# Kernel tuning notes

Measured on AMD Instinct MI355X. Metric: run time of the kernel, lower is better.

The kernel has to match this reference:

```python
import jax, jax.numpy as jnp
import numpy as np

HIDDEN = 2048
N_HEADS = 32
N_KV_HEADS = 8
N_GROUPS = N_HEADS // N_KV_HEADS  # 4
HEAD_DIM = HIDDEN // N_HEADS      # 64
BATCH, SEQ = 2, 2048


def setup_inputs() -> dict:
    key = jax.random.key(0)
    ks = jax.random.split(key, 5)
    s = 0.02
    return {
        "x": jax.random.normal(ks[0], (BATCH, SEQ, HIDDEN), dtype=jnp.float32),
        "Wq": jax.random.normal(ks[1], (HIDDEN, HIDDEN), dtype=jnp.float32) * s,
        "Wk": jax.random.normal(ks[2], (N_KV_HEADS * HEAD_DIM, HIDDEN), dtype=jnp.float32) * s,
        "Wv": jax.random.normal(ks[3], (N_KV_HEADS * HEAD_DIM, HIDDEN), dtype=jnp.float32) * s,
        "Wo": jax.random.normal(ks[4], (HIDDEN, HIDDEN), dtype=jnp.float32) * s,
    }


def reference(x, Wq, Wk, Wv, Wo):
    b, s, _ = x.shape
    # Projections (nn.Linear: y = x @ W.T)
    q = (x @ Wq.T).reshape(b, s, N_KV_HEADS, N_GROUPS, HEAD_DIM)  # group heads by kv head
    k = (x @ Wk.T).reshape(b, s, N_KV_HEADS, HEAD_DIM)
    v = (x @ Wv.T).reshape(b, s, N_KV_HEADS, HEAD_DIM)
    scale = 1.0 / jnp.sqrt(jnp.asarray(HEAD_DIM, dtype=x.dtype))
    # Grouped scores: equivalent to repeat_interleave of K over groups
    scores = jnp.einsum('bqhgd,bkhd->bhgqk', q, k) * scale  # [b, kvh, g, s, s]
    causal_mask = jnp.triu(jnp.ones((s, s), dtype=bool), k=1)
    scores = jnp.where(causal_mask, -jnp.inf, scores)
    attn = jax.nn.softmax(scores, axis=-1)
    out = jnp.einsum('bhgqk,bkhd->bqhgd', attn, v)  # [b, s, kvh, g, hd]
    out = out.reshape(b, s, HIDDEN)
    return out @ Wo.T
```

## Files before the change

kernel.cpp:

```cpp
#include <hip/hip_runtime.h>

#define HIDDEN 2048
#define NHEADS 32
#define NKV 8
#define HD 64
#define BATCH 2
#define SEQ 2048
#define MROWS (BATCH*SEQ)
#define KVDIM (NKV*HD)
#define QKVN (HIDDEN + 2*KVDIM)

typedef __bf16 bf16x8 __attribute__((ext_vector_type(8)));
typedef __bf16 bf16x4 __attribute__((ext_vector_type(4)));
typedef float f32x4 __attribute__((ext_vector_type(4)));

__device__ inline f32x4 mfma32(bf16x8 a, bf16x8 b, f32x4 c) {
    return __builtin_amdgcn_mfma_f32_16x16x32_bf16(a, b, c, 0, 0, 0);
}

__device__ inline void gld16(const __bf16* g, __bf16* l) {
    __builtin_amdgcn_global_load_lds((const __attribute__((address_space(1))) void*)g,
                                     (__attribute__((address_space(3))) void*)l, 16, 0, 0);
}

__global__ __launch_bounds__(256) void cast_all(const float* __restrict__ x,
                                                const float* __restrict__ wq,
                                                const float* __restrict__ wk,
                                                const float* __restrict__ wv,
                                                const float* __restrict__ wo,
                                                __bf16* __restrict__ xb,
                                                __bf16* __restrict__ wqkv,
                                                __bf16* __restrict__ wob,
                                                float qscale) {
    int blk = blockIdx.x;
    const float* src; __bf16* dst; float sc = 1.0f; size_t off;
    if (blk < 8192)        { src = x;  dst = xb;   off = (size_t)blk * 1024; }
    else if (blk < 12288)  { src = wq; dst = wqkv; off = (size_t)(blk - 8192) * 1024; sc = qscale; }
    else if (blk < 13312)  { src = wk; dst = wqkv + (size_t)HIDDEN * HIDDEN; off = (size_t)(blk - 12288) * 1024; }
    else if (blk < 14336)  { src = wv; dst = wqkv + (size_t)(HIDDEN + KVDIM) * HIDDEN; off = (size_t)(blk - 13312) * 1024; }
    else                   { src = wo; dst = wob;  off = (size_t)(blk - 14336) * 1024; }
    size_t i4 = off + (size_t)threadIdx.x * 4;
    float4 f = *(const float4*)(src + i4);
    dst[i4 + 0] = (__bf16)(f.x * sc);
    dst[i4 + 1] = (__bf16)(f.y * sc);
    dst[i4 + 2] = (__bf16)(f.z * sc);
    dst[i4 + 3] = (__bf16)(f.w * sc);
}

__device__ inline void store_val(__bf16* C, size_t idx, float v) { C[idx] = (__bf16)v; }
__device__ inline void store_val(float* C, size_t idx, float v) { C[idx] = v; }

template <typename OutT>
__global__ __launch_bounds__(256) void gemm128(const __bf16* __restrict__ A,
                                               const __bf16* __restrict__ B,
                                               OutT* __restrict__ C,
                                               int M, int N, int K) {
    __shared__ __bf16 As[2][128][32];
    __shared__ __bf16 Bs[2][128][32];
    const int tid  = threadIdx.x;
    const int lane = tid & 63;
    const int w    = tid >> 6;
    const int col  = lane & 15;
    const int quad = lane >> 4;
    const int m0 = blockIdx.y * 128;
    const int n0 = blockIdx.x * 128;
    const int wm = (w >> 1) * 64;
    const int wn = (w & 1) * 64;

    f32x4 acc[4][4];
    #pragma unroll
    for (int i = 0; i < 4; i++)
        #pragma unroll
        for (int j = 0; j < 4; j++) acc[i][j] = (f32x4){0.f,0.f,0.f,0.f};

    const int lrow = lane >> 2;
    const int lcol = (lane & 3) * 8;

    auto stage = [&](int k0, int buf) {
        #pragma unroll
        for (int c = 0; c < 4; c++) {
            int chunk = w * 4 + c;
            if (chunk < 8) {
                const __bf16* g = A + (size_t)(m0 + chunk*16 + lrow) * K + k0 + lcol;
                gld16(g, &As[buf][chunk*16][0]);
            } else {
                int bc = chunk - 8;
                const __bf16* g = B + (size_t)(n0 + bc*16 + lrow) * K + k0 + lcol;
                gld16(g, &Bs[buf][bc*16][0]);
            }
        }
    };

    const int nk = K / 32;
    stage(0, 0);
    for (int ki = 0; ki < nk; ki++) {
        const int buf = ki & 1;
        __syncthreads();
        if (ki + 1 < nk) stage((ki + 1) * 32, buf ^ 1);

        bf16x8 af[4], bfr[4];
        #pragma unroll
        for (int i = 0; i < 4; i++) af[i]  = *(const bf16x8*)&As[buf][wm + i*16 + col][quad*8];
        #pragma unroll
        for (int j = 0; j < 4; j++) bfr[j] = *(const bf16x8*)&Bs[buf][wn + j*16 + col][quad*8];
        #pragma unroll
        for (int i = 0; i < 4; i++)
            #pragma unroll
            for (int j = 0; j < 4; j++)
                acc[i][j] = __builtin_amdgcn_mfma_f32_16x16x32_bf16(af[i], bfr[j], acc[i][j], 0, 0, 0);
    }

    #pragma unroll
    for (int i = 0; i < 4; i++) {
        #pragma unroll
        for (int r = 0; r < 4; r++) {
            int mrow = m0 + wm + i*16 + quad*4 + r;
            size_t base = (size_t)mrow * N + n0 + wn;
            #pragma unroll
            for (int j = 0; j < 4; j++)
                store_val(C, base + j*16 + col, acc[i][j][r]);
        }
    }
}

__global__ __launch_bounds__(256) void transpose_v(const __bf16* __restrict__ QKV,
                                                   __bf16* __restrict__ VT) {
    __shared__ __bf16 tile[64][72];
    const int r0 = blockIdx.x * 64;
    const int s0 = blockIdx.y * 64;
    const int t  = threadIdx.x;
    #pragma unroll
    for (int cc = 0; cc < 2; cc++) {
        int c = t + cc * 256;
        int i = c >> 3;
        int j8 = (c & 7) * 8;
        bf16x8 v = *(const bf16x8*)(QKV + (size_t)(s0 + i) * QKVN + (HIDDEN + KVDIM) + r0 + j8);
        *(bf16x8*)&tile[i][j8] = v;
    }
    __syncthreads();
    #pragma unroll
    for (int cc = 0; cc < 2; cc++) {
        int c = t + cc * 256;
        int d = c >> 3;
        int m = c & 7;
        bf16x8 vv;
        #pragma unroll
        for (int tt = 0; tt < 8; tt++) {
            int sl = (m >> 2) * 32 + (tt >> 2) * 16 + (m & 3) * 4 + (tt & 3);
            vv[tt] = tile[sl][d];
        }
        *(bf16x8*)(VT + (size_t)(r0 + d) * MROWS + s0 + m * 8) = vv;
    }
}

__global__ __launch_bounds__(256) void flash_attn(const __bf16* __restrict__ QKV,
                                                  const __bf16* __restrict__ VT,
                                                  __bf16* __restrict__ O) {
    const int bid  = blockIdx.x;
    const int t    = 31 - (bid >> 6);
    const int head = (bid >> 1) & 31;
    const int b    = bid & 1;
    const int kvh  = head >> 2;
    const int tid  = threadIdx.x;
    const int lane = tid & 63;
    const int w    = tid >> 6;
    const int col  = lane & 15;
    const int quad = lane >> 4;

    const int qb   = t * 64 + w * 16;
    const int n32  = (t + 1) * 2;

    __shared__ __bf16 Ks[3][2][32][32];
    __shared__ __bf16 Vs[3][64][32];

    const size_t qO = (size_t)(b * SEQ + qb + col) * QKVN + head * HD;
    bf16x8 aq0 = *(const bf16x8*)(QKV + qO + quad * 8);
    bf16x8 aq1 = *(const bf16x8*)(QKV + qO + 32 + quad * 8);

    bf16x8 ones8;
    #pragma unroll
    for (int j = 0; j < 8; j++) ones8[j] = (__bf16)1.0f;

    f32x4 o[4];
    #pragma unroll
    for (int dn = 0; dn < 4; dn++) o[dn] = (f32x4){0.f,0.f,0.f,0.f};
    f32x4 lsum = (f32x4){0.f,0.f,0.f,0.f};

    const int lrow = lane >> 2;
    const int srcc8 = (((lane & 3) ^ (lrow & 3)) * 8);
    const int swz   = (quad ^ (col & 3)) * 8;
    const size_t bS = (size_t)b * SEQ;

    const __bf16 *g0, *g1;
    size_t gstep;
    if (w < 2) {
        g0 = QKV + (bS + lrow) * QKVN + HIDDEN + kvh * HD + w * 32 + srcc8;
        g1 = g0 + (size_t)16 * QKVN;
        gstep = (size_t)32 * QKVN;
    } else {
        g0 = VT + (size_t)(kvh * HD + (w - 2) * 32 + lrow) * MROWS + bS + (lane & 3) * 8;
        g1 = g0 + (size_t)16 * MROWS;
        gstep = 32;
    }

    auto stage = [&](int sb) {
        if (w < 2) {
            gld16(g0, &Ks[sb][w][0][0]);
            gld16(g1, &Ks[sb][w][16][0]);
        } else {
            gld16(g0, &Vs[sb][(w - 2) * 32][0]);
            gld16(g1, &Vs[sb][(w - 2) * 32 + 16][0]);
        }
        g0 += gstep; g1 += gstep;
    };

    stage(0);
    stage(1);
    int cur = 0, nx2 = 2;
    for (int kt = 0; kt < n32; kt++) {
        const int kbase = kt * 32;
        if (kt + 1 < n32) { __asm__ volatile("s_waitcnt vmcnt(2)" ::: "memory"); }
        else              { __asm__ volatile("s_waitcnt vmcnt(0)" ::: "memory"); }
        __builtin_amdgcn_s_barrier();
        __asm__ volatile("" ::: "memory");
        if (kt + 2 < n32) stage(nx2);

        f32x4 s[2];
        s[0] = (f32x4){0.f,0.f,0.f,0.f};
        s[1] = (f32x4){0.f,0.f,0.f,0.f};
        __builtin_amdgcn_s_setprio(1);
        #pragma unroll
        for (int j = 0; j < 2; j++) {
            bf16x8 bk0 = *(const bf16x8*)&Ks[cur][0][j*16 + col][swz];
            bf16x8 bk1 = *(const bf16x8*)&Ks[cur][1][j*16 + col][swz];
            s[j] = mfma32(bk0, aq0, s[j]);
            s[j] = mfma32(bk1, aq1, s[j]);
        }
        __builtin_amdgcn_s_setprio(0);

        if (kt >= n32 - 2) {
            #pragma unroll
            for (int j = 0; j < 2; j++)
                #pragma unroll
                for (int r = 0; r < 4; r++)
                    if (kbase + j*16 + quad*4 + r > qb + col) s[j][r] = -1e30f;
        }

        bf16x8 pa;
        #pragma unroll
        for (int j = 0; j < 2; j++)
            #pragma unroll
            for (int r = 0; r < 4; r++)
                pa[j*4 + r] = (__bf16)__builtin_amdgcn_exp2f(s[j][r]);

        __builtin_amdgcn_s_setprio(1);
        lsum = mfma32(pa, ones8, lsum);
        #pragma unroll
        for (int dn = 0; dn < 4; dn++) {
            bf16x8 bv = *(const bf16x8*)&Vs[cur][dn*16 + col][quad*8];
            o[dn] = mfma32(pa, bv, o[dn]);
        }
        __builtin_amdgcn_s_setprio(0);

        cur = (cur == 2) ? 0 : cur + 1;
        nx2 = (nx2 == 2) ? 0 : nx2 + 1;
    }

    #pragma unroll
    for (int r = 0; r < 4; r++) {
        float inv = 1.0f / lsum[r];
        __bf16* op = O + (size_t)(b * SEQ + qb + quad*4 + r) * HIDDEN + head * HD;
        #pragma unroll
        for (int dn = 0; dn < 4; dn++)
            op[dn*16 + col] = (__bf16)(o[dn][r] * inv);
    }
}

extern "C" void kernel_launch(void* const* d_in, const int* in_sizes, int n_in,
                              void* d_out, int out_size, void* d_ws, size_t ws_size,
                              hipStream_t stream) {
    const float* x  = (const float*)d_in[0];
    const float* Wq = (const float*)d_in[1];
    const float* Wk = (const float*)d_in[2];
    const float* Wv = (const float*)d_in[3];
    const float* Wo = (const float*)d_in[4];
    float* out = (float*)d_out;

    __bf16* p    = (__bf16*)d_ws;
    __bf16* xb   = p; p += (size_t)MROWS * HIDDEN;
    __bf16* wqkv = p; p += (size_t)QKVN * HIDDEN;
    __bf16* wob  = p; p += (size_t)HIDDEN * HIDDEN;
    __bf16* qkv  = p; p += (size_t)MROWS * QKVN;
    __bf16* vt   = p; p += (size_t)KVDIM * MROWS;
    __bf16* aob  = xb;

    const float qscale = 0.125f * 1.4426950408889634f;
    cast_all<<<18432, 256, 0, stream>>>(x, Wq, Wk, Wv, Wo, xb, wqkv, wob, qscale);

    dim3 blk(256);
    gemm128<__bf16><<<dim3(QKVN/128, MROWS/128), blk, 0, stream>>>(xb, wqkv, qkv, MROWS, QKVN, HIDDEN);
    transpose_v<<<dim3(KVDIM/64, MROWS/64), blk, 0, stream>>>(qkv, vt);
    flash_attn<<<BATCH * NHEADS * (SEQ/64), blk, 0, stream>>>(qkv, vt, aob);
    gemm128<float><<<dim3(HIDDEN/128, MROWS/128), blk, 0, stream>>>(aob, wob, out, MROWS, HIDDEN, HIDDEN);
}
```

Before: 283.9 us.

## Add 256x256 pipelined GEMM with 8 waves for QKV projection

Adds a new gemm256 kernel for the fused QKV projection. It uses 256x256 output tiles, 512 threads, double-buffered LDS filled by direct global-to-LDS loads with XOR swizzling, and an interleaved schedule of LDS reads, MFMA and prefetch issues with explicit waitcnt, barriers and s_setprio. Larger tiles raise reuse per loaded byte and the software pipeline is meant to hide load latency. The grid becomes small (12x16 = 192 blocks), which may underfill the GPU, and the hand-tuned vmcnt counts carry correctness risk.

```diff
diff --git a/kernel.cpp b/kernel.cpp
--- a/kernel.cpp
+++ b/kernel.cpp
@@ -123,6 +123,131 @@
     }
 }
 
+__global__ __launch_bounds__(512, 2) void gemm256(const __bf16* __restrict__ A,
+                                                  const __bf16* __restrict__ B,
+                                                  __bf16* __restrict__ C,
+                                                  int M, int N, int K) {
+    __shared__ __bf16 As[2][256][64];
+    __shared__ __bf16 Bs[2][256][64];
+    const int tid  = threadIdx.x;
+    const int lane = tid & 63;
+    const int w    = tid >> 6;
+    const int wr   = w >> 2;
+    const int wc   = w & 3;
+    const int col  = lane & 15;
+    const int quad = lane >> 4;
+    const int m0 = blockIdx.y * 256;
+    const int n0 = blockIdx.x * 256;
+    const int nk = K >> 6;
+
+    f32x4 acc[8][4];
+    #pragma unroll
+    for (int i = 0; i < 8; i++)
+        #pragma unroll
+        for (int j = 0; j < 4; j++) acc[i][j] = (f32x4){0.f,0.f,0.f,0.f};
+
+    bf16x8 afr[4][2];
+    bf16x8 bfr[4][2];
+
+    const int r8 = lane >> 3, c8 = lane & 7;
+    const __bf16* pA0 = A + (size_t)(m0 + w*16 +     r8) * K + ((c8 ^ quad) * 8);
+    const __bf16* pA1 = A + (size_t)(m0 + w*16 + 8 + r8) * K + ((c8 ^ (4 + quad)) * 8);
+    const __bf16* pB0 = B + (size_t)(n0 + w*16 +     r8) * K + ((c8 ^ quad) * 8);
+    const __bf16* pB1 = B + (size_t)(n0 + w*16 + 8 + r8) * K + ((c8 ^ (4 + quad)) * 8);
+    const int ldsrow = w * 16;
+    const int rsw = col >> 1;
+
+#define G2_BAR()   { __asm__ volatile("" ::: "memory"); __builtin_amdgcn_s_barrier(); __asm__ volatile("" ::: "memory"); }
+#define G2_LGKM0() { __asm__ volatile("s_waitcnt lgkmcnt(0)" ::: "memory"); __builtin_amdgcn_sched_barrier(0); }
+#define G2_ISSUE(tile, sel) do {                                                             \
+    int _t = (tile);                                                                         \
+    if (_t < nk) {                                                                           \
+        int _b = _t & 1; size_t _ko = (size_t)_t * 64;                                       \
+        if      ((sel) == 0) { gld16(pA0 + _ko, &As[_b][ldsrow][0]);                         \
+                               gld16(pA1 + _ko, &As[_b][ldsrow + 8][0]); }                   \
+        else if ((sel) == 1) { gld16(pA0 + (size_t)128*K + _ko, &As[_b][128 + ldsrow][0]);   \
+                               gld16(pA1 + (size_t)128*K + _ko, &As[_b][128 + ldsrow + 8][0]); } \
+        else if ((sel) == 2) { gld16(pB0 + _ko, &Bs[_b][ldsrow][0]);                         \
+                               gld16(pB1 + _ko, &Bs[_b][ldsrow + 8][0]); }                   \
+        else                 { gld16(pB0 + (size_t)128*K + _ko, &Bs[_b][128 + ldsrow][0]);   \
+                               gld16(pB1 + (size_t)128*K + _ko, &Bs[_b][128 + ldsrow + 8][0]); } \
+    } } while (0)
+#define G2_LDA(mh) {                                                                         \
+    _Pragma("unroll")                                                                        \
+    for (int ii = 0; ii < 4; ii++) {                                                         \
+        const __bf16* _rp = &As[buf][wr*128 + ((mh)*4 + ii)*16 + col][0];                    \
+        _Pragma("unroll")                                                                    \
+        for (int kk = 0; kk < 2; kk++)                                                       \
+            afr[ii][kk] = *(const bf16x8*)(_rp + (((kk*4 + quad) ^ rsw) * 8));               \
+    } }
+#define G2_LDB(nh) {                                                                         \
+    _Pragma("unroll")                                                                        \
+    for (int jj = 0; jj < 2; jj++) {                                                         \
+        const __bf16* _rp = &Bs[buf][wc*64 + ((nh)*2 + jj)*16 + col][0];                     \
+        _Pragma("unroll")                                                                    \
+        for (int kk = 0; kk < 2; kk++)                                                       \
+            bfr[(nh)*2 + jj][kk] = *(const bf16x8*)(_rp + (((kk*4 + quad) ^ rsw) * 8));      \
+    } }
+#define G2_MM(mh, nh) {                                                                      \
+    __builtin_amdgcn_s_setprio(1);                                                           \
+    _Pragma("unroll")                                                                        \
+    for (int ii = 0; ii < 4; ii++)                                                           \
+        _Pragma("unroll")                                                                    \
+        for (int jj = 0; jj < 2; jj++)                                                       \
+            _Pragma("unroll")                                                                \
+            for (int kk = 0; kk < 2; kk++)                                                   \
+                acc[(mh)*4 + ii][(nh)*2 + jj] =                                              \
+                    mfma32(afr[ii][kk], bfr[(nh)*2 + jj][kk], acc[(mh)*4 + ii][(nh)*2 + jj]); \
+    __builtin_amdgcn_s_setprio(0); }
+
+    G2_ISSUE(0, 0); G2_ISSUE(0, 1); G2_ISSUE(0, 2); G2_ISSUE(0, 3);
+    G2_ISSUE(1, 0); G2_ISSUE(1, 2); G2_ISSUE(1, 3);
+    __asm__ volatile("s_waitcnt vmcnt(6)" ::: "memory");
+    G2_BAR();
+
+    for (int t = 0; t < nk; ++t) {
+        const int buf = t & 1;
+        G2_LDA(0); G2_LDB(0);
+        G2_ISSUE(t + 1, 1);
+        G2_BAR(); G2_LGKM0();
+        G2_MM(0, 0);
+        G2_BAR();
+        G2_LDB(1);
+        G2_BAR(); G2_LGKM0();
+        G2_MM(0, 1);
+        G2_BAR();
+        G2_LDA(1);
+        G2_ISSUE(t + 2, 2);
+        G2_BAR(); G2_LGKM0();
+        G2_MM(1, 1);
+        G2_BAR();
+        G2_ISSUE(t + 2, 0);
+        G2_ISSUE(t + 2, 3);
+        G2_BAR(); G2_LGKM0();
+        G2_MM(1, 0);
+        if (t + 3 <= nk) { __asm__ volatile("s_waitcnt vmcnt(6)" ::: "memory"); }
+        else             { __asm__ volatile("s_waitcnt vmcnt(0)" ::: "memory"); }
+        G2_BAR();
+    }
+
+    #pragma unroll
+    for (int i16 = 0; i16 < 8; i16++) {
+        #pragma unroll
+        for (int r = 0; r < 4; r++) {
+            size_t base = (size_t)(m0 + wr*128 + i16*16 + quad*4 + r) * N + n0 + wc*64;
+            #pragma unroll
+            for (int j16 = 0; j16 < 4; j16++)
+                C[base + j16*16 + col] = (__bf16)acc[i16][j16][r];
+        }
+    }
+#undef G2_BAR
+#undef G2_LGKM0
+#undef G2_ISSUE
+#undef G2_LDA
+#undef G2_LDB
+#undef G2_MM
+}
+
 __global__ __launch_bounds__(256) void transpose_v(const __bf16* __restrict__ QKV,
                                                    __bf16* __restrict__ VT) {
     __shared__ __bf16 tile[64][72];
@@ -297,9 +422,8 @@
     const float qscale = 0.125f * 1.4426950408889634f;
     cast_all<<<18432, 256, 0, stream>>>(x, Wq, Wk, Wv, Wo, xb, wqkv, wob, qscale);
 
-    dim3 blk(256);
-    gemm128<__bf16><<<dim3(QKVN/128, MROWS/128), blk, 0, stream>>>(xb, wqkv, qkv, MROWS, QKVN, HIDDEN);
-    transpose_v<<<dim3(KVDIM/64, MROWS/64), blk, 0, stream>>>(qkv, vt);
-    flash_attn<<<BATCH * NHEADS * (SEQ/64), blk, 0, stream>>>(qkv, vt, aob);
-    gemm128<float><<<dim3(HIDDEN/128, MROWS/128), blk, 0, stream>>>(aob, wob, out, MROWS, HIDDEN, HIDDEN);
-}
+    gemm256<<<dim3(QKVN/256, MROWS/256), 512, 0, stream>>>(xb, wqkv, qkv, MROWS, QKVN, HIDDEN);
+    transpose_v<<<dim3(KVDIM/64, MROWS/64), dim3(256), 0, stream>>>(qkv, vt);
+    flash_attn<<<BATCH * NHEADS * (SEQ/64), dim3(256), 0, stream>>>(qkv, vt, aob);
+    gemm128<float><<<dim3(HIDDEN/128, MROWS/128), dim3(256), 0, stream>>>(aob, wob, out, MROWS, HIDDEN, HIDDEN);
+}
```

After: 280.0 us. About the same (-1.4%).

## Use 256x192-tile double-buffered GEMM for the fused QKV projection

Applied to the files above, without the earlier changes.

Adds a new 512-thread GEMM kernel for the QKV projection. It uses 256x192 output tiles, double-buffered LDS filled by direct global-to-LDS loads, XOR-swizzled LDS reads, and MFMA issue interleaved with register prefetch under s_setprio. The larger tile raises arithmetic intensity and the software pipelining overlaps loads with MFMAs, aiming to speed up the QKV GEMM. QKVN=3072 divides evenly by 192 into 16 column blocks, giving 256 blocks in total. The cost is heavier register and LDS use per block.

```diff
diff --git a/kernel.cpp b/kernel.cpp
--- a/kernel.cpp
+++ b/kernel.cpp
@@ -123,6 +123,145 @@
     }
 }
 
+__global__ __launch_bounds__(512, 2) void gemm256(const __bf16* __restrict__ A,
+                                                  const __bf16* __restrict__ B,
+                                                  __bf16* __restrict__ C,
+                                                  int M, int N, int K) {
+    __shared__ __bf16 As[2][256][64];
+    __shared__ __bf16 Bs[2][192][64];
+    const int tid  = threadIdx.x;
+    const int lane = tid & 63;
+    const int w    = tid >> 6;
+    const int wr   = w >> 2;
+    const int wc   = w & 3;
+    const int col  = lane & 15;
+    const int quad = lane >> 4;
+    const int m0 = blockIdx.y * 256;
+    const int n0 = blockIdx.x * 192;
+    const int nk = K >> 6;
+
+    f32x4 acc[8][3];
+    #pragma unroll
+    for (int i = 0; i < 8; i++)
+        #pragma unroll
+        for (int j = 0; j < 3; j++) acc[i][j] = (f32x4){0.f,0.f,0.f,0.f};
+
+    bf16x8 amh0[4][2];
+    bf16x8 amh1[4][2];
+    bf16x8 b01[2][2];
+    bf16x8 b2v[2];
+
+    const int r8 = lane >> 3, c8 = lane & 7;
+    const __bf16* pA0 = A + (size_t)(m0 + w*16 +     r8) * K + ((c8 ^ quad) * 8);
+    const __bf16* pA1 = A + (size_t)(m0 + w*16 + 8 + r8) * K + ((c8 ^ (4 + quad)) * 8);
+    const __bf16* pB  = B + (size_t)(n0 + w*8 +      r8) * K + ((c8 ^ ((w & 1) * 4 + quad)) * 8);
+    const int rsw = col >> 1;
+
+    auto issue = [&](int tt) {
+        if (tt < nk) {
+            int b = tt & 1; size_t ko = (size_t)tt * 64;
+            gld16(pA0 + ko,                  &As[b][w*16][0]);
+            gld16(pA1 + ko,                  &As[b][w*16 + 8][0]);
+            gld16(pA0 + (size_t)128*K + ko,  &As[b][128 + w*16][0]);
+            gld16(pA1 + (size_t)128*K + ko,  &As[b][128 + w*16 + 8][0]);
+            gld16(pB + ko,                   &Bs[b][w*8][0]);
+            gld16(pB + (size_t)64*K + ko,    &Bs[b][64 + w*8][0]);
+            gld16(pB + (size_t)128*K + ko,   &Bs[b][128 + w*8][0]);
+        }
+    };
+    auto rdA = [&](bf16x8 (&dst)[4][2], int b, int rowbase) {
+        #pragma unroll
+        for (int i = 0; i < 4; i++) {
+            const __bf16* rp = &As[b][rowbase + i*16 + col][0];
+            #pragma unroll
+            for (int kk = 0; kk < 2; kk++)
+                dst[i][kk] = *(const bf16x8*)(rp + (((kk*4 + quad) ^ rsw) * 8));
+        }
+    };
+    auto rdB01 = [&](int b) {
+        #pragma unroll
+        for (int j = 0; j < 2; j++) {
+            const __bf16* rp = &Bs[b][wc*48 + j*16 + col][0];
+            #pragma unroll
+            for (int kk = 0; kk < 2; kk++)
+                b01[j][kk] = *(const bf16x8*)(rp + (((kk*4 + quad) ^ rsw) * 8));
+        }
+    };
+
+    issue(0); issue(1);
+    __asm__ volatile("s_waitcnt vmcnt(7)" ::: "memory");
+    __builtin_amdgcn_s_barrier();
+    __asm__ volatile("" ::: "memory");
+    rdA(amh0, 0, wr*128);
+    rdB01(0);
+
+    for (int t = 0; t < nk; ++t) {
+        const int buf = t & 1;
+        {
+            const __bf16* rp = &Bs[buf][wc*48 + 32 + col][0];
+            #pragma unroll
+            for (int kk = 0; kk < 2; kk++)
+                b2v[kk] = *(const bf16x8*)(rp + (((kk*4 + quad) ^ rsw) * 8));
+        }
+        __builtin_amdgcn_s_setprio(1);
+        #pragma unroll
+        for (int i = 0; i < 4; i++)
+            #pragma unroll
+            for (int j = 0; j < 2; j++)
+                #pragma unroll
+                for (int kk = 0; kk < 2; kk++)
+                    acc[i][j] = mfma32(amh0[i][kk], b01[j][kk], acc[i][j]);
+        __builtin_amdgcn_s_setprio(0);
+        rdA(amh1, buf, wr*128 + 64);
+        __builtin_amdgcn_s_setprio(1);
+        #pragma unroll
+        for (int i = 0; i < 4; i++)
+            #pragma unroll
+            for (int kk = 0; kk < 2; kk++)
+                acc[i][2] = mfma32(amh0[i][kk], b2v[kk], acc[i][2]);
+        __builtin_amdgcn_s_setprio(0);
+        __builtin_amdgcn_s_setprio(1);
+        #pragma unroll
+        for (int i = 0; i < 4; i++)
+            #pragma unroll
+            for (int j = 0; j < 2; j++)
+                #pragma unroll
+                for (int kk = 0; kk < 2; kk++)
+                    acc[4+i][j] = mfma32(amh1[i][kk], b01[j][kk], acc[4+i][j]);
+        __builtin_amdgcn_s_setprio(0);
+
+        __asm__ volatile("s_waitcnt vmcnt(0) lgkmcnt(0)" ::: "memory");
+        __builtin_amdgcn_sched_barrier(0);
+        __builtin_amdgcn_s_barrier();
+        __asm__ volatile("" ::: "memory");
+
+        if (t + 1 < nk) {
+            rdA(amh0, buf ^ 1, wr*128);
+            rdB01(buf ^ 1);
+        }
+        issue(t + 2);
+
+        __builtin_amdgcn_s_setprio(1);
+        #pragma unroll
+        for (int i = 0; i < 4; i++)
+            #pragma unroll
+            for (int kk = 0; kk < 2; kk++)
+                acc[4+i][2] = mfma32(amh1[i][kk], b2v[kk], acc[4+i][2]);
+        __builtin_amdgcn_s_setprio(0);
+    }
+
+    #pragma unroll
+    for (int i16 = 0; i16 < 8; i16++) {
+        #pragma unroll
+        for (int r = 0; r < 4; r++) {
+            size_t base = (size_t)(m0 + wr*128 + i16*16 + quad*4 + r) * N + n0 + wc*48;
+            #pragma unroll
+            for (int j = 0; j < 3; j++)
+                C[base + j*16 + col] = (__bf16)acc[i16][j][r];
+        }
+    }
+}
+
 __global__ __launch_bounds__(256) void transpose_v(const __bf16* __restrict__ QKV,
                                                    __bf16* __restrict__ VT) {
     __shared__ __bf16 tile[64][72];
@@ -297,9 +436,8 @@
     const float qscale = 0.125f * 1.4426950408889634f;
     cast_all<<<18432, 256, 0, stream>>>(x, Wq, Wk, Wv, Wo, xb, wqkv, wob, qscale);
 
-    dim3 blk(256);
-    gemm128<__bf16><<<dim3(QKVN/128, MROWS/128), blk, 0, stream>>>(xb, wqkv, qkv, MROWS, QKVN, HIDDEN);
-    transpose_v<<<dim3(KVDIM/64, MROWS/64), blk, 0, stream>>>(qkv, vt);
-    flash_attn<<<BATCH * NHEADS * (SEQ/64), blk, 0, stream>>>(qkv, vt, aob);
-    gemm128<float><<<dim3(HIDDEN/128, MROWS/128), blk, 0, stream>>>(aob, wob, out, MROWS, HIDDEN, HIDDEN);
-}
+    gemm256<<<dim3(QKVN/192, MROWS/256), 512, 0, stream>>>(xb, wqkv, qkv, MROWS, QKVN, HIDDEN);
+    transpose_v<<<dim3(KVDIM/64, MROWS/64), dim3(256), 0, stream>>>(qkv, vt);
+    flash_attn<<<BATCH * NHEADS * (SEQ/64), dim3(256), 0, stream>>>(qkv, vt, aob);
+    gemm128<float><<<dim3(HIDDEN/128, MROWS/128), dim3(256), 0, stream>>>(aob, wob, out, MROWS, HIDDEN, HIDDEN);
+}
```

Result: faster. 271.7 us (-4.3%).
